# Optimization experiments

Measured on AMD Instinct MI355X. Metric: run time of the kernel, lower is better.

## Reference

```python
import jax, jax.numpy as jnp
import numpy as np

NEG_INF = jnp.float32(-jnp.inf)


def setup_inputs() -> dict:
    key = jax.random.key(0)
    k1, k2, k3, k4 = jax.random.split(key, 4)
    B, QL, H = 16, 32, 128          # batch, query tokens, embed dim
    N_DOCS, DL = 20000, 64          # documents, doc tokens per doc
    N_CAND = 1024                   # candidate embeddings per query
    N_EMB = N_DOCS * DL
    return {
        "q_vectors": jax.random.normal(k1, (B, QL, H), dtype=jnp.float32),
        "topk_indices": jax.random.randint(k2, (B, N_CAND), 0, N_EMB, dtype=jnp.int64),
        "vectors": jax.random.normal(k3, (N_DOCS, DL, H), dtype=jnp.float32),
        "emb2pid": jax.random.randint(k4, (N_EMB,), 0, N_DOCS, dtype=jnp.int64),
        "k": 100,
    }


def _dedup_pids(pids):
    # Emulate MaxSimPartition._get_unique_pids: unique pids per row, invalid -> -1.
    # Sort descending so any -1 entries go last, then mark duplicates as -1.
    s = -jnp.sort(-pids, axis=1)                              # [b, n] descending
    dup = jnp.concatenate(
        [jnp.zeros((s.shape[0], 1), dtype=bool), s[:, 1:] == s[:, :-1]], axis=1
    )
    return jnp.where(dup, -1, s)


def reference(q_vectors, topk_indices, vectors, emb2pid, k):
    # Map retrieved embedding rows to document pids (single partition, boundary 0).
    pids = emb2pid[topk_indices]                              # [b, n]
    n_docs = vectors.shape[0]
    pids = jnp.where((pids < 0) | (pids >= n_docs), -1, pids)
    pids = _dedup_pids(pids)                                  # [b, n]

    # Gather doc-token vectors and compute MaxSim:
    # max over doc tokens, mean over query tokens.
    d_vectors = vectors[jnp.clip(pids, 0)]                    # [b, n, d, h]
    sim = jnp.einsum("bqh,bndh->bnqd", q_vectors, d_vectors)  # [b, n, q, d]
    scores = sim.max(axis=-1).mean(axis=-1)                   # [b, n]
    scores = jnp.where(pids < 0, NEG_INF, scores)

    # Merge/top-k (single partition => one final top-k).
    k_ = min(int(k), scores.shape[-1])
    top_scores, idx = jax.lax.top_k(scores.astype(jnp.float32), k_)
    top_pids = jnp.take_along_axis(pids, idx, axis=1)
    return top_pids, top_scores
```

## Files before the change

kernel.cpp:

```cpp
#include <hip/hip_runtime.h>
#include <hip/hip_bf16.h>
#include <math.h>

#define BB   16
#define NC   1024
#define QL   32
#define HD   128
#define DLN  64
#define RK   128
#define NPW  2

typedef __attribute__((ext_vector_type(8))) short bf16x8;
typedef __attribute__((ext_vector_type(4))) float f32x4;
typedef __attribute__((ext_vector_type(4))) double f64x4;

__global__ __launch_bounds__(256) void k_qprep(
    const float* __restrict__ q, unsigned short* __restrict__ qhi)
{
    int i = blockIdx.x * 256 + threadIdx.x;
    float v = q[i];
    __hip_bfloat16 h = __float2bfloat16(v);
    qhi[i] = *reinterpret_cast<unsigned short*>(&h);
}

__global__ __launch_bounds__(1024) void k_gather_sort_dedup(
    const int* __restrict__ topk, const int* __restrict__ emb2pid,
    int n_emb, int n_docs, int* __restrict__ pids_out)
{
    const int b = blockIdx.x;
    const int t = threadIdx.x;
    __shared__ int s[NC];

    int idx = topk[b * NC + t];
    int pid = (idx >= 0 && idx < n_emb) ? emb2pid[idx] : -1;
    if (pid < 0 || pid >= n_docs) pid = -1;
    s[t] = pid;
    __syncthreads();

    for (int k2 = 2; k2 <= NC; k2 <<= 1) {
        for (int j = k2 >> 1; j > 0; j >>= 1) {
            int ixj = t ^ j;
            if (ixj > t) {
                int a = s[t], c = s[ixj];
                bool desc = ((t & k2) == 0);
                if (desc ? (a < c) : (a > c)) { s[t] = c; s[ixj] = a; }
            }
            __syncthreads();
        }
    }
    int v = s[t];
    pids_out[b * NC + t] = (t > 0 && v == s[t - 1]) ? -1 : v;
}

__device__ __forceinline__ bf16x8 cvt8(float4 a, float4 c)
{
    float v[8] = {a.x, a.y, a.z, a.w, c.x, c.y, c.z, c.w};
    bf16x8 r;
#pragma unroll
    for (int j = 0; j < 8; ++j) {
        __hip_bfloat16 h = __float2bfloat16(v[j]);
        r[j] = *reinterpret_cast<short*>(&h);
    }
    return r;
}

__global__ __launch_bounds__(256, 4) void k_screen_mfma(
    const unsigned short* __restrict__ qhi,
    const float* __restrict__ vecs,
    const int* __restrict__ pids,
    float* __restrict__ scores)
{
    const int lane = threadIdx.x & 63;
    const int wv   = threadIdx.x >> 6;
    const int bk   = blockIdx.x;
    const int BPR  = NC / (4 * NPW);
    const int b    = bk / BPR;
    const int nb   = (bk % BPR) * (4 * NPW) + wv * NPW;

    const int r16 = lane & 15;
    const int kb  = lane >> 4;

    bf16x8 qf[2][4];
#pragma unroll
    for (int m = 0; m < 2; ++m)
#pragma unroll
        for (int ks = 0; ks < 4; ++ks) {
            int off = ((b * QL + m * 16 + r16) * HD + ks * 32 + kb * 8);
            qf[m][ks] = *(const bf16x8*)(qhi + off);
        }

    for (int nn = 0; nn < NPW; ++nn) {
        const int n = nb + nn;
        const int pid = pids[b * NC + n];
        if (pid < 0) {
            if (lane == 0) scores[b * NC + n] = -__builtin_inff();
            continue;
        }
        const float* dbase = vecs + (size_t)pid * (DLN * HD);

        f32x4 acc[2][4] = {};
#pragma unroll
        for (int ks = 0; ks < 4; ++ks) {
#pragma unroll
            for (int nt = 0; nt < 4; ++nt) {
                const float* p = dbase + (nt * 16 + r16) * HD + ks * 32 + kb * 8;
                float4 x0 = *(const float4*)p;
                float4 x1 = *(const float4*)(p + 4);
                bf16x8 bh = cvt8(x0, x1);
#pragma unroll
                for (int m = 0; m < 2; ++m)
                    acc[m][nt] = __builtin_amdgcn_mfma_f32_16x16x32_bf16(
                        qf[m][ks], bh, acc[m][nt], 0, 0, 0);
            }
        }

        float s = 0.f;
#pragma unroll
        for (int m = 0; m < 2; ++m) {
#pragma unroll
            for (int r = 0; r < 4; ++r) {
                float x = fmaxf(fmaxf(acc[m][0][r], acc[m][1][r]),
                                fmaxf(acc[m][2][r], acc[m][3][r]));
                x = fmaxf(x, __shfl_xor(x, 1));
                x = fmaxf(x, __shfl_xor(x, 2));
                x = fmaxf(x, __shfl_xor(x, 4));
                x = fmaxf(x, __shfl_xor(x, 8));
                s += x;
            }
        }
        s += __shfl_xor(s, 16);
        s += __shfl_xor(s, 32);
        if (lane == 0) scores[b * NC + n] = s * (1.0f / 32.0f);
    }
}

__global__ __launch_bounds__(1024) void k_select(
    const float* __restrict__ scores, int* __restrict__ sel)
{
    const int b = blockIdx.x;
    const int t = threadIdx.x;
    __shared__ float ss[NC];
    __shared__ int   si[NC];

    ss[t] = scores[b * NC + t];
    si[t] = t;
    __syncthreads();

    for (int k2 = 2; k2 <= NC; k2 <<= 1) {
        for (int j = k2 >> 1; j > 0; j >>= 1) {
            int ixj = t ^ j;
            if (ixj > t) {
                float as = ss[t], bs = ss[ixj];
                int   ai = si[t], bi = si[ixj];
                bool a_first = (as > bs) || (as == bs && ai < bi);
                bool desc = ((t & k2) == 0);
                if (desc ? !a_first : a_first) { ss[t] = bs; si[t] = bi; ss[ixj] = as; si[ixj] = ai; }
            }
            __syncthreads();
        }
    }
    if (t < RK) sel[b * RK + t] = si[t];
}

#define DPAD (HD + 4)

__global__ __launch_bounds__(256) void k_rescore_mfma(
    const float* __restrict__ q,
    const float* __restrict__ vecs,
    const int* __restrict__ pids,
    const int* __restrict__ sel,
    double* __restrict__ resc)
{
    const int r = blockIdx.x, b = blockIdx.y;
    const int t = threadIdx.x;
    const int n = sel[b * RK + r];
    const int pid = pids[b * NC + n];
    if (pid < 0) {
        if (t == 0) resc[b * RK + r] = -__builtin_inf();
        return;
    }

    __shared__ float  sq[QL][DPAD];
    __shared__ float  sdoc[DLN][DPAD];
    __shared__ double red[4][QL];

    {
        const float4* src = (const float4*)(q + (size_t)b * QL * HD);
        for (int i = t; i < QL * HD / 4; i += 256) {
            int row = i >> 5, c4 = (i & 31) << 2;
            *(float4*)&sq[row][c4] = src[i];
        }
    }
    {
        const float4* src = (const float4*)(vecs + (size_t)pid * DLN * HD);
        for (int i = t; i < DLN * HD / 4; i += 256) {
            int row = i >> 5, c4 = (i & 31) << 2;
            *(float4*)&sdoc[row][c4] = src[i];
        }
    }
    __syncthreads();

    const int lane = t & 63;
    const int wv   = t >> 6;
    const int c16  = lane & 15;
    const int kq   = lane >> 4;

    f64x4 acc[2] = {};
#pragma unroll 4
    for (int ks = 0; ks < 32; ++ks) {
        double bv = (double)sdoc[wv * 16 + c16][ks * 4 + kq];
        double a0 = (double)sq[c16][ks * 4 + kq];
        double a1 = (double)sq[16 + c16][ks * 4 + kq];
        acc[0] = __builtin_amdgcn_mfma_f64_16x16x4f64(a0, bv, acc[0], 0, 0, 0);
        acc[1] = __builtin_amdgcn_mfma_f64_16x16x4f64(a1, bv, acc[1], 0, 0, 0);
    }

#pragma unroll
    for (int m = 0; m < 2; ++m)
#pragma unroll
        for (int rr = 0; rr < 4; ++rr) {
            double x = acc[m][rr];
            x = fmax(x, __shfl_xor(x, 1));
            x = fmax(x, __shfl_xor(x, 2));
            x = fmax(x, __shfl_xor(x, 4));
            x = fmax(x, __shfl_xor(x, 8));
            if (c16 == 0) red[wv][m * 16 + kq * 4 + rr] = x;
        }
    __syncthreads();

    if (t < 32) {
        double v = fmax(fmax(red[0][t], red[1][t]), fmax(red[2][t], red[3][t]));
        v += __shfl_xor(v, 1);
        v += __shfl_xor(v, 2);
        v += __shfl_xor(v, 4);
        v += __shfl_xor(v, 8);
        v += __shfl_xor(v, 16);
        if (t == 0) resc[b * RK + r] = v * (1.0 / 32.0);
    }
}

__global__ __launch_bounds__(RK) void k_final(
    const double* __restrict__ resc, const int* __restrict__ sel,
    const int* __restrict__ pids, float* __restrict__ out, int k)
{
    const int b = blockIdx.x;
    const int t = threadIdx.x;
    __shared__ double ss[RK];
    __shared__ int    sn[RK];

    ss[t] = resc[b * RK + t];
    sn[t] = sel[b * RK + t];
    __syncthreads();

    for (int k2 = 2; k2 <= RK; k2 <<= 1) {
        for (int j = k2 >> 1; j > 0; j >>= 1) {
            int ixj = t ^ j;
            if (ixj > t) {
                double as = ss[t], bs = ss[ixj];
                int    ai = sn[t], bi = sn[ixj];
                bool a_first = (as > bs) || (as == bs && ai < bi);
                bool desc = ((t & k2) == 0);
                if (desc ? !a_first : a_first) { ss[t] = bs; sn[t] = bi; ss[ixj] = as; sn[ixj] = ai; }
            }
            __syncthreads();
        }
    }

    if (t < k) {
        out[b * k + t]          = (float)pids[b * NC + sn[t]];
        out[BB * k + b * k + t] = (float)ss[t];
    }
}

extern "C" void kernel_launch(void* const* d_in, const int* in_sizes, int n_in,
                              void* d_out, int out_size, void* d_ws, size_t ws_size,
                              hipStream_t stream)
{
    const float* q_vectors = (const float*)d_in[0];
    const int*   topk_idx  = (const int*)d_in[1];
    const float* vectors   = (const float*)d_in[2];
    const int*   emb2pid   = (const int*)d_in[3];

    const int n_emb  = in_sizes[3];
    const int n_docs = in_sizes[2] / (DLN * HD);
    const int k      = out_size / (2 * BB);

    char* ws = (char*)d_ws;
    int*    pids_ws   = (int*)ws;      ws += BB * NC * sizeof(int);
    float*  scores_ws = (float*)ws;    ws += BB * NC * sizeof(float);
    int*    sel_ws    = (int*)ws;      ws += BB * RK * sizeof(int);
    double* resc_ws   = (double*)ws;   ws += BB * RK * sizeof(double);
    unsigned short* qhi_ws = (unsigned short*)ws;

    k_qprep<<<dim3(BB * QL * HD / 256), dim3(256), 0, stream>>>(
        q_vectors, qhi_ws);

    k_gather_sort_dedup<<<dim3(BB), dim3(NC), 0, stream>>>(
        topk_idx, emb2pid, n_emb, n_docs, pids_ws);

    k_screen_mfma<<<dim3(BB * NC / (4 * NPW)), dim3(256), 0, stream>>>(
        qhi_ws, vectors, pids_ws, scores_ws);

    k_select<<<dim3(BB), dim3(NC), 0, stream>>>(scores_ws, sel_ws);

    k_rescore_mfma<<<dim3(RK, BB), dim3(256), 0, stream>>>(
        q_vectors, vectors, pids_ws, sel_ws, resc_ws);

    k_final<<<dim3(BB), dim3(RK), 0, stream>>>(
        resc_ws, sel_ws, pids_ws, (float*)d_out, k);
}
```

Before: 167.6 us.

## Restructure screen kernel with double-buffered LDS doc staging and cross-wave reduction

```diff
diff --git a/kernel.cpp b/kernel.cpp
--- a/kernel.cpp
+++ b/kernel.cpp
@@ -8,7 +8,7 @@
 #define HD   128
 #define DLN  64
 #define RK   128
-#define NPW  2
+#define CPB  32
 
 typedef __attribute__((ext_vector_type(8))) short bf16x8;
 typedef __attribute__((ext_vector_type(4))) float f32x4;
@@ -52,33 +52,46 @@
     pids_out[b * NC + t] = (t > 0 && v == s[t - 1]) ? -1 : v;
 }
 
-__device__ __forceinline__ bf16x8 cvt8(float4 a, float4 c)
-{
-    float v[8] = {a.x, a.y, a.z, a.w, c.x, c.y, c.z, c.w};
-    bf16x8 r;
-#pragma unroll
-    for (int j = 0; j < 8; ++j) {
-        __hip_bfloat16 h = __float2bfloat16(v[j]);
-        r[j] = *reinterpret_cast<short*>(&h);
-    }
-    return r;
-}
-
-__global__ __launch_bounds__(256, 4) void k_screen_mfma(
+__device__ __forceinline__ bf16x8 cvt8_rtz(float4 a, float4 b)
+{
+    union { unsigned int u[4]; bf16x8 v; } r;
+    r.u[0] = __builtin_amdgcn_perm(__float_as_uint(a.y), __float_as_uint(a.x), 0x07060302u);
+    r.u[1] = __builtin_amdgcn_perm(__float_as_uint(a.w), __float_as_uint(a.z), 0x07060302u);
+    r.u[2] = __builtin_amdgcn_perm(__float_as_uint(b.y), __float_as_uint(b.x), 0x07060302u);
+    r.u[3] = __builtin_amdgcn_perm(__float_as_uint(b.w), __float_as_uint(b.z), 0x07060302u);
+    return r.v;
+}
+
+__global__ __launch_bounds__(256, 2) void k_screen_mfma(
     const unsigned short* __restrict__ qhi,
     const float* __restrict__ vecs,
     const int* __restrict__ pids,
     float* __restrict__ scores)
 {
-    const int lane = threadIdx.x & 63;
-    const int wv   = threadIdx.x >> 6;
-    const int bk   = blockIdx.x;
-    const int BPR  = NC / (4 * NPW);
-    const int b    = bk / BPR;
-    const int nb   = (bk % BPR) * (4 * NPW) + wv * NPW;
-
-    const int r16 = lane & 15;
-    const int kb  = lane >> 4;
+    const int t    = threadIdx.x;
+    const int lane = t & 63;
+    const int wv   = t >> 6;
+    const int blk  = blockIdx.x;
+    const int b    = blk >> 5;
+    const int n0   = (blk & 31) * CPB;
+
+    __shared__ float sdoc[2][DLN * HD];
+    __shared__ float red[2][4][QL];
+
+    const int pid_l = pids[b * NC + n0 + (lane & 31)];
+
+    int soff[8];
+#pragma unroll
+    for (int j = 0; j < 8; ++j) {
+        int rd = wv * 16 + j * 2 + (lane >> 5);
+        int c  = (lane & 31) ^ (rd & 7);
+        soff[j] = (rd * 32 + c) * 4;
+    }
+
+    const int r16   = lane & 15;
+    const int kb    = lane >> 4;
+    const int rbase = (wv * 16 + r16) * HD;
+    const int rx    = (r16 & 7) * 4;
 
     bf16x8 qf[2][4];
 #pragma unroll
@@ -88,49 +101,75 @@
             int off = ((b * QL + m * 16 + r16) * HD + ks * 32 + kb * 8);
             qf[m][ks] = *(const bf16x8*)(qhi + off);
         }
-
-    for (int nn = 0; nn < NPW; ++nn) {
-        const int n = nb + nn;
-        const int pid = pids[b * NC + n];
-        if (pid < 0) {
-            if (lane == 0) scores[b * NC + n] = -__builtin_inff();
-            continue;
-        }
-        const float* dbase = vecs + (size_t)pid * (DLN * HD);
-
-        f32x4 acc[2][4] = {};
+    asm volatile("s_waitcnt vmcnt(0)" ::: "memory");
+
+    {
+        int pid0 = __shfl(pid_l, 0);
+        const float* dbase = vecs + (size_t)(pid0 < 0 ? 0 : pid0) * (DLN * HD);
+#pragma unroll
+        for (int j = 0; j < 8; ++j)
+            __builtin_amdgcn_global_load_lds(
+                (const __attribute__((address_space(1))) void*)(dbase + soff[j]),
+                (__attribute__((address_space(3))) void*)(&sdoc[0][wv * 2048 + j * 256]),
+                16, 0, 0);
+    }
+
+    for (int i = 0; i < CPB; ++i) {
+        const int cur = i & 1;
+
+        if (i + 1 < CPB) {
+            int pid1 = __shfl(pid_l, i + 1);
+            const float* dbase = vecs + (size_t)(pid1 < 0 ? 0 : pid1) * (DLN * HD);
+#pragma unroll
+            for (int j = 0; j < 8; ++j)
+                __builtin_amdgcn_global_load_lds(
+                    (const __attribute__((address_space(1))) void*)(dbase + soff[j]),
+                    (__attribute__((address_space(3))) void*)(&sdoc[cur ^ 1][wv * 2048 + j * 256]),
+                    16, 0, 0);
+            asm volatile("s_waitcnt vmcnt(8)" ::: "memory");
+        } else {
+            asm volatile("s_waitcnt vmcnt(0)" ::: "memory");
+        }
+
+        const float* dbuf = &sdoc[cur][0];
+        f32x4 acc[2] = {};
 #pragma unroll
         for (int ks = 0; ks < 4; ++ks) {
-#pragma unroll
-            for (int nt = 0; nt < 4; ++nt) {
-                const float* p = dbase + (nt * 16 + r16) * HD + ks * 32 + kb * 8;
-                float4 x0 = *(const float4*)p;
-                float4 x1 = *(const float4*)(p + 4);
-                bf16x8 bh = cvt8(x0, x1);
-#pragma unroll
-                for (int m = 0; m < 2; ++m)
-                    acc[m][nt] = __builtin_amdgcn_mfma_f32_16x16x32_bf16(
-                        qf[m][ks], bh, acc[m][nt], 0, 0, 0);
-            }
-        }
-
-        float s = 0.f;
-#pragma unroll
-        for (int m = 0; m < 2; ++m) {
+            int o0 = rbase + ((ks * 32 + kb * 8) ^ rx);
+            float4 x0 = *(const float4*)(dbuf + o0);
+            float4 x1 = *(const float4*)(dbuf + (o0 ^ 4));
+            bf16x8 bh = cvt8_rtz(x0, x1);
+            acc[0] = __builtin_amdgcn_mfma_f32_16x16x32_bf16(qf[0][ks], bh, acc[0], 0, 0, 0);
+            acc[1] = __builtin_amdgcn_mfma_f32_16x16x32_bf16(qf[1][ks], bh, acc[1], 0, 0, 0);
+        }
+
+#pragma unroll
+        for (int m = 0; m < 2; ++m)
 #pragma unroll
             for (int r = 0; r < 4; ++r) {
-                float x = fmaxf(fmaxf(acc[m][0][r], acc[m][1][r]),
-                                fmaxf(acc[m][2][r], acc[m][3][r]));
+                float x = acc[m][r];
                 x = fmaxf(x, __shfl_xor(x, 1));
                 x = fmaxf(x, __shfl_xor(x, 2));
                 x = fmaxf(x, __shfl_xor(x, 4));
                 x = fmaxf(x, __shfl_xor(x, 8));
-                s += x;
+                if (r16 == 0) red[cur][wv][m * 16 + kb * 4 + r] = x;
             }
-        }
-        s += __shfl_xor(s, 16);
-        s += __shfl_xor(s, 32);
-        if (lane == 0) scores[b * NC + n] = s * (1.0f / 32.0f);
+        asm volatile("s_waitcnt lgkmcnt(0)" ::: "memory");
+        __builtin_amdgcn_s_barrier();
+
+        if (t < 32) {
+            float v = fmaxf(fmaxf(red[cur][0][t], red[cur][1][t]),
+                            fmaxf(red[cur][2][t], red[cur][3][t]));
+            v += __shfl_xor(v, 1);
+            v += __shfl_xor(v, 2);
+            v += __shfl_xor(v, 4);
+            v += __shfl_xor(v, 8);
+            v += __shfl_xor(v, 16);
+            int pidi = __shfl(pid_l, i);
+            if (t == 0)
+                scores[b * NC + n0 + i] =
+                    (pidi < 0) ? -__builtin_inff() : v * (1.0f / 32.0f);
+        }
     }
 }
 
@@ -298,7 +337,7 @@
     k_gather_sort_dedup<<<dim3(BB), dim3(NC), 0, stream>>>(
         topk_idx, emb2pid, n_emb, n_docs, pids_ws);
 
-    k_screen_mfma<<<dim3(BB * NC / (4 * NPW)), dim3(256), 0, stream>>>(
+    k_screen_mfma<<<dim3(BB * NC / CPB), dim3(256), 0, stream>>>(
         qhi_ws, vectors, pids_ws, scores_ws);
 
     k_select<<<dim3(BB), dim3(NC), 0, stream>>>(scores_ws, sel_ws);
```

After: 179.7 us. 7.2% more time.
